# Kernel tuning notes

Hardware: AMD Instinct MI355X
Metric: run time of the kernel (lower is better)

The kernel has to match this reference:

```python
import jax, jax.numpy as jnp
import numpy as np

# Static tree-slice layout from TeaBlock.call:
# 15 windows of width 256 with stride 128 starting at 0, plus one window [1820:2176] (width 356).
_STARTS = np.arange(15) * 128  # starts for cores 1..15
_WIN_IDX = _STARTS[:, None] + np.arange(256)[None, :]  # (15, 256)
NUM_CLS = 10
NUM_OUT = round(256 / NUM_CLS) * NUM_CLS  # 260


def setup_inputs() -> dict:
    key = jax.random.key(0)
    ks = jax.random.split(key, 9)
    B = 16384
    s = 0.05
    return {
        "x":   jax.random.normal(ks[0], (B, 2176), dtype=jnp.float32),
        "W1":  jax.random.normal(ks[1], (15, 256, 64), dtype=jnp.float32) * s,
        "b1":  jnp.zeros((15, 64), dtype=jnp.float32),
        "W16": jax.random.normal(ks[2], (356, 64), dtype=jnp.float32) * s,
        "b16": jnp.zeros((64,), dtype=jnp.float32),
        "W2":  jax.random.normal(ks[3], (4, 256, 64), dtype=jnp.float32) * s,
        "b2":  jnp.zeros((4, 64), dtype=jnp.float32),
        "W3":  jax.random.normal(ks[4], (256, NUM_OUT), dtype=jnp.float32) * s,
        "b3":  jnp.zeros((NUM_OUT,), dtype=jnp.float32),
    }


def _tea(x, W, b):
    # Tea layer = constrained dense + ReLU (SNN-style accumulate-and-fire unit)
    return jax.nn.relu(x @ W + b)


def reference(x, W1, b1, W16, b16, W2, b2, W3, b3):
    B = x.shape[0]
    xf = x.reshape(B, -1)[:, :2176]
    # --- level 1: 15 regular strided windows, batched as one einsum ---
    xwin = xf[:, _WIN_IDX]                                   # (B, 15, 256)
    y15 = jax.nn.relu(jnp.einsum("bks,kso->bko", xwin, W1) + b1)  # (B, 15, 64)
    # core_1_16 on the irregular window [1820:2176]
    y16 = _tea(xf[:, 1820:2176], W16, b16)                   # (B, 64)
    # concat in original order x1..x16 -> (B, 1024), grouped 4-at-a-time into 256
    y = jnp.concatenate([y15.reshape(B, 15 * 64), y16], axis=1)  # (B, 1024)
    g = y.reshape(B, 4, 256)
    # --- level 2: 4 Tea(64), batched ---
    z = jax.nn.relu(jnp.einsum("bks,kso->bko", g, W2) + b2)  # (B, 4, 64)
    z = z.reshape(B, 256)
    # --- level 3: Tea(260) ---
    h = _tea(z, W3, b3)                                      # (B, 260)
    # AdditivePooling: sum NUM_OUT//NUM_CLS units per class
    pooled = h.reshape(B, NUM_CLS, NUM_OUT // NUM_CLS).sum(axis=2)  # (B, 10)
    return jax.nn.softmax(pooled, axis=-1)
```

## Files before the change

kernel.cpp:

```cpp
#include <hip/hip_runtime.h>
#include <cstdint>
#include <cstddef>

typedef _Float16 f16x8 __attribute__((ext_vector_type(8)));
typedef _Float16 f16x4 __attribute__((ext_vector_type(4)));
typedef float    f32x4 __attribute__((ext_vector_type(4)));

#define MFMA16(a,b,c) __builtin_amdgcn_mfma_f32_16x16x32_f16((a),(b),(c),0,0,0)

__global__ void tea_prep(const float* __restrict__ W1, const float* __restrict__ W16,
                         const float* __restrict__ W2, const float* __restrict__ W3,
                         _Float16* __restrict__ ws)
{
    int i = blockIdx.x * blockDim.x + threadIdx.x;
    if (i < 245760) {
        int win = i >> 14, t = i & 16383;
        int ot = t >> 12, kk = (t >> 9) & 7, l = (t >> 3) & 63, j = t & 7;
        int o = 16 * ot + (l & 15);
        int s = 32 * kk + 8 * (l >> 4) + j;
        ws[i] = (_Float16)W1[(win * 256 + s) * 64 + o];
    } else if (i < 270336) {
        int t = i - 245760;
        int ot = t / 6144, t2 = t % 6144;
        int kk = t2 >> 9, l = (t2 >> 3) & 63, j = t2 & 7;
        int o = 16 * ot + (l & 15);
        int sp = 32 * kk + 8 * (l >> 4) + j;
        ws[i] = (_Float16)((sp >= 12 && sp < 368) ? W16[(sp - 12) * 64 + o] : 0.f);
    } else if (i < 335872) {
        int t = i - 270336;
        int q2 = t >> 12, kk = (t >> 9) & 7, l = (t >> 3) & 63, j = t & 7;
        int og = 16 * q2 + (l & 15);
        int g = q2 >> 2, o2 = og - 64 * g;
        int s = 32 * kk + 8 * (l >> 4) + j;
        ws[i] = (_Float16)W2[(g * 256 + s) * 64 + o2];
    } else if (i < 405504) {
        int t = i - 335872;
        int tt = t >> 12, kk = (t >> 9) & 7, l = (t >> 3) & 63, j = t & 7;
        int o = 16 * tt + (l & 15);
        int s = 32 * kk + 8 * (l >> 4) + j;
        ws[i] = (_Float16)((o < 260) ? W3[s * 260 + o] : 0.f);
    }
}

__global__ __launch_bounds__(1024, 4)
void tea_dma(const float* __restrict__ x,
             const float* __restrict__ b1,  const float* __restrict__ b16,
             const float* __restrict__ b2,  const float* __restrict__ b3,
             const _Float16* __restrict__ ws, float* __restrict__ out)
{
    __shared__ _Float16 sh[74240];
    char* shb = (char*)sh;

    const int tid = threadIdx.x;
    const int bid = blockIdx.x;
    const int wg  = (bid & 7) * 64 + (bid >> 3);
    const int q = tid >> 6, l = tid & 63, r = l & 15, kg = l >> 4;
    const bool prod = (q >= 8);
    const int  pw   = q - 8;

    const char* xb = (const char*)(x + (size_t)wg * 32 * 2176);

    auto issue = [&](int c) {
        #pragma unroll
        for (int i = 0; i < 2; ++i) {
            int row = 4 * pw + 2 * i + (l >> 5);
            int colphys = (l & 31) * 16;
            int collog = colphys ^ ((row & 7) << 4);
            const void* src = xb + (size_t)row * 8704 + (size_t)c * 512 + collog;
            void* dst = shb + (c % 7) * 16384 + (4 * pw + 2 * i) * 512;
            __builtin_amdgcn_global_load_lds(
                (const __attribute__((address_space(1))) void*)src,
                (__attribute__((address_space(3))) void*)dst, 16, 0, 0);
        }
    };

#define PASSTOP(N) do { \
    if (prod) asm volatile("s_waitcnt vmcnt(" #N ")" ::: "memory"); \
    asm volatile("s_waitcnt lgkmcnt(0)" ::: "memory"); \
    __builtin_amdgcn_s_barrier(); \
    __builtin_amdgcn_sched_barrier(0); } while (0)
#define BARL() do { \
    asm volatile("s_waitcnt lgkmcnt(0)" ::: "memory"); \
    __builtin_amdgcn_s_barrier(); \
    __builtin_amdgcn_sched_barrier(0); } while (0)

    auto bfrag = [&](int slotbyte, int rowloc, int colb) -> f16x8 {
        int swz = (rowloc & 7) << 4;
        f32x4 u = *(const f32x4*)(shb + slotbyte + rowloc * 512 + (colb ^ swz));
        f32x4 v = *(const f32x4*)(shb + slotbyte + rowloc * 512 + ((colb + 16) ^ swz));
        f16x8 B;
        B[0] = (_Float16)u[0]; B[1] = (_Float16)u[1]; B[2] = (_Float16)u[2]; B[3] = (_Float16)u[3];
        B[4] = (_Float16)v[0]; B[5] = (_Float16)v[1]; B[6] = (_Float16)v[2]; B[7] = (_Float16)v[3];
        return B;
    };

    f16x8 Afn[8];
    if (!prod) {
        const _Float16* A0 = ws + (q >> 2) * 16384 + (q & 3) * 4096;
        #pragma unroll
        for (int kk = 0; kk < 8; ++kk)
            Afn[kk] = *(const f16x8*)(A0 + kk * 512 + l * 8);
    }

    auto wincomp2 = [&](int win, const float* bp, int nextwin) {
        float4 bv = *(const float4*)(bp + 16 * (q & 3) + 4 * kg);
        f32x4 acc0 = {0.f, 0.f, 0.f, 0.f}, acc1 = {0.f, 0.f, 0.f, 0.f};
        __builtin_amdgcn_s_setprio(1);
        #pragma unroll
        for (int kk = 0; kk < 8; ++kk) {
            int slotb = ((win + (kk >> 2)) % 7) * 16384;
            int colb = 128 * (kk & 3) + 32 * kg;
            f16x8 B0 = bfrag(slotb, r, colb);
            f16x8 B1 = bfrag(slotb, 16 + r, colb);
            acc0 = MFMA16(Afn[kk], B0, acc0);
            acc1 = MFMA16(Afn[kk], B1, acc1);
        }
        __builtin_amdgcn_s_setprio(0);
        if (nextwin >= 0) {
            const _Float16* An = ws + nextwin * 16384 + (q & 3) * 4096;
            #pragma unroll
            for (int kk = 0; kk < 8; ++kk)
                Afn[kk] = *(const f16x8*)(An + kk * 512 + l * 8);
        }
        f16x4 pk0, pk1;
        pk0[0] = (_Float16)fmaxf(acc0[0] + bv.x, 0.f);
        pk0[1] = (_Float16)fmaxf(acc0[1] + bv.y, 0.f);
        pk0[2] = (_Float16)fmaxf(acc0[2] + bv.z, 0.f);
        pk0[3] = (_Float16)fmaxf(acc0[3] + bv.w, 0.f);
        pk1[0] = (_Float16)fmaxf(acc1[0] + bv.x, 0.f);
        pk1[1] = (_Float16)fmaxf(acc1[1] + bv.y, 0.f);
        pk1[2] = (_Float16)fmaxf(acc1[2] + bv.z, 0.f);
        pk1[3] = (_Float16)fmaxf(acc1[3] + bv.w, 0.f);
        *(f16x4*)&sh[57344 + r * 264 + 64 * (win & 3) + 16 * (q & 3) + 4 * kg] = pk0;
        *(f16x4*)&sh[57344 + (16 + r) * 264 + 64 * (win & 3) + 16 * (q & 3) + 4 * kg] = pk1;
    };

    auto y16comp = [&](int rh) {
        const _Float16* A = ws + 245760 + (q & 3) * 6144;
        const int rowloc = 16 * rh + r;
        f32x4 acc = {0.f, 0.f, 0.f, 0.f};
        #pragma unroll
        for (int kk = 0; kk < 12; ++kk) {
            int off32 = 16 + 32 * kk + 8 * kg;
            if (32 * kk + 8 * kg >= 368) off32 = 376;
            int cc = off32 >> 7;
            int slotb = cc * 16384;
            int colb = (off32 & 127) * 4;
            f16x8 B  = bfrag(slotb, rowloc, colb);
            f16x8 Af = *(const f16x8*)(A + kk * 512 + l * 8);
            acc = MFMA16(Af, B, acc);
        }
        float4 bv = *(const float4*)(b16 + 16 * (q & 3) + 4 * kg);
        f16x4 pk;
        pk[0] = (_Float16)fmaxf(acc[0] + bv.x, 0.f);
        pk[1] = (_Float16)fmaxf(acc[1] + bv.y, 0.f);
        pk[2] = (_Float16)fmaxf(acc[2] + bv.z, 0.f);
        pk[3] = (_Float16)fmaxf(acc[3] + bv.w, 0.f);
        *(f16x4*)&sh[57344 + rowloc * 264 + 192 + 16 * (q & 3) + 4 * kg] = pk;
    };

    auto l2group = [&](int g) {
        if (q < 8) {
            int rh = q >> 2, t = 4 * g + (q & 3);
            const _Float16* A = ws + 270336 + t * 4096;
            f32x4 acc = {0.f, 0.f, 0.f, 0.f};
            #pragma unroll
            for (int kk = 0; kk < 8; ++kk) {
                f16x8 B  = *(const f16x8*)&sh[57344 + (16 * rh + r) * 264 + 32 * kk + 8 * kg];
                f16x8 Af = *(const f16x8*)(A + kk * 512 + l * 8);
                acc = MFMA16(Af, B, acc);
            }
            float4 bv = *(const float4*)(b2 + 16 * t + 4 * kg);
            f16x4 pk;
            pk[0] = (_Float16)fmaxf(acc[0] + bv.x, 0.f);
            pk[1] = (_Float16)fmaxf(acc[1] + bv.y, 0.f);
            pk[2] = (_Float16)fmaxf(acc[2] + bv.z, 0.f);
            pk[3] = (_Float16)fmaxf(acc[3] + bv.w, 0.f);
            *(f16x4*)&sh[65792 + (16 * rh + r) * 264 + 16 * t + 4 * kg] = pk;
        }
    };

    if (prod) { issue(0); issue(1); issue(2); issue(3); issue(4); }

    {
        const int wq = q >> 2;
        PASSTOP(4);
        if (prod) { issue(5); issue(6); }
        else      wincomp2(0 + wq, b1 + (0 + wq) * 64, 2 + wq);
        PASSTOP(4);
        if (prod) { issue(7); issue(8); }
        else      wincomp2(2 + wq, b1 + (2 + wq) * 64, 4 + wq);
        BARL(); l2group(0);
        PASSTOP(4);
        if (prod) { issue(9); issue(10); }
        else      wincomp2(4 + wq, b1 + (4 + wq) * 64, 6 + wq);
        PASSTOP(4);
        if (prod) { issue(11); issue(12); }
        else      wincomp2(6 + wq, b1 + (6 + wq) * 64, 8 + wq);
        BARL(); l2group(1);
        PASSTOP(4);
        if (prod) { issue(13); issue(14); }
        else      wincomp2(8 + wq, b1 + (8 + wq) * 64, 10 + wq);
        PASSTOP(4);
        if (prod) { issue(15); issue(16); }
        else      wincomp2(10 + wq, b1 + (10 + wq) * 64, 12 + wq);
        BARL(); l2group(2);
        PASSTOP(4);
        if (!prod) wincomp2(12 + wq, b1 + (12 + wq) * 64, -1);
        PASSTOP(0);
        if (!prod) {
            {
                const _Float16* A = ws + 14 * 16384 + (q & 3) * 4096;
                const int rh = q >> 2, rowloc = 16 * rh + r;
                f32x4 acc = {0.f, 0.f, 0.f, 0.f};
                #pragma unroll
                for (int kk = 0; kk < 8; ++kk) {
                    int slotb = ((14 + (kk >> 2)) % 7) * 16384;
                    int colb = 128 * (kk & 3) + 32 * kg;
                    f16x8 Af = *(const f16x8*)(A + kk * 512 + l * 8);
                    acc = MFMA16(Af, bfrag(slotb, rowloc, colb), acc);
                }
                float4 bv = *(const float4*)(b1 + 14 * 64 + 16 * (q & 3) + 4 * kg);
                f16x4 pk;
                pk[0] = (_Float16)fmaxf(acc[0] + bv.x, 0.f);
                pk[1] = (_Float16)fmaxf(acc[1] + bv.y, 0.f);
                pk[2] = (_Float16)fmaxf(acc[2] + bv.z, 0.f);
                pk[3] = (_Float16)fmaxf(acc[3] + bv.w, 0.f);
                *(f16x4*)&sh[57344 + rowloc * 264 + 64 * (14 & 3) + 16 * (q & 3) + 4 * kg] = pk;
            }
            y16comp(q >> 2);
        }
        BARL(); l2group(3);
    }
    BARL();

    {
        float* psp = (float*)sh;
        auto l3job = [&](int t, int rh2) {
            const _Float16* A = ws + 335872 + t * 4096;
            f32x4 acc = {0.f, 0.f, 0.f, 0.f};
            #pragma unroll
            for (int kk = 0; kk < 8; ++kk) {
                f16x8 B  = *(const f16x8*)&sh[65792 + (16 * rh2 + r) * 264 + 32 * kk + 8 * kg];
                f16x8 Af = *(const f16x8*)(A + kk * 512 + l * 8);
                acc = MFMA16(Af, B, acc);
            }
            float p[10];
            #pragma unroll
            for (int c = 0; c < 10; ++c) p[c] = 0.f;
            #pragma unroll
            for (int tt = 0; tt < 4; ++tt) {
                int o = 16 * t + 4 * kg + tt;
                if (o < 260) p[(unsigned)o / 26u] += fmaxf(acc[tt] + b3[o], 0.f);
            }
            #pragma unroll
            for (int c = 0; c < 10; ++c) {
                p[c] += __shfl_xor(p[c], 16);
                p[c] += __shfl_xor(p[c], 32);
            }
            if (kg == 0) {
                #pragma unroll
                for (int c = 0; c < 10; ++c)
                    psp[t * 320 + (16 * rh2 + r) * 10 + c] = p[c];
            }
        };
        l3job(q >> 1, q & 1);
        l3job((q + 16) >> 1, q & 1);
        if (q < 2) l3job(16, q);
    }
    BARL();

    if (tid < 32) {
        const float* psp = (const float*)sh;
        float v[10];
        #pragma unroll
        for (int c = 0; c < 10; ++c) {
            float s = 0.f;
            #pragma unroll
            for (int t = 0; t < 17; ++t) s += psp[t * 320 + tid * 10 + c];
            v[c] = s;
        }
        float mx = v[0];
        #pragma unroll
        for (int c = 1; c < 10; ++c) mx = fmaxf(mx, v[c]);
        float e[10], se = 0.f;
        #pragma unroll
        for (int c = 0; c < 10; ++c) { e[c] = expf(v[c] - mx); se += e[c]; }
        float inv = 1.f / se;
        float* orow = out + (size_t)(wg * 32 + tid) * 10;
        #pragma unroll
        for (int c = 0; c < 10; ++c) orow[c] = e[c] * inv;
    }
#undef PASSTOP
#undef BARL
}

extern "C" void kernel_launch(void* const* d_in, const int* in_sizes, int n_in,
                              void* d_out, int out_size, void* d_ws, size_t ws_size,
                              hipStream_t stream)
{
    const float* x   = (const float*)d_in[0];
    const float* W1  = (const float*)d_in[1];
    const float* b1  = (const float*)d_in[2];
    const float* W16 = (const float*)d_in[3];
    const float* b16 = (const float*)d_in[4];
    const float* W2  = (const float*)d_in[5];
    const float* b2  = (const float*)d_in[6];
    const float* W3  = (const float*)d_in[7];
    const float* b3  = (const float*)d_in[8];
    float*    out = (float*)d_out;
    _Float16* ws  = (_Float16*)d_ws;

    tea_prep<<<1584, 256, 0, stream>>>(W1, W16, W2, W3, ws);
    tea_dma <<<512, 1024, 0, stream>>>(x, b1, b16, b2, b3, ws, out);
}
```

Measured before the change: 62.35 us.

## Stage x through registers as fp16 and double rows per workgroup

Replaces the direct global-to-LDS async fp32 copies with register loads by producer waves that convert to fp16 before writing swizzled LDS slots. The fp16 staging halves LDS footprint per chunk, so each workgroup now processes 64 rows instead of 32 with a 5-slot ring, launching 256 blocks instead of 512. Intent is to cut LDS read and conversion work per MFMA and to reuse each weight fragment across four row tiles. The cost is an extra barrier-synchronised register stage, fewer blocks, and loss of the async DMA overlap.

Measured after the change: 51.18 us. 1.22x faster.

```diff
diff --git a/kernel.cpp b/kernel.cpp
--- a/kernel.cpp
+++ b/kernel.cpp
@@ -48,72 +48,82 @@
              const float* __restrict__ b2,  const float* __restrict__ b3,
              const _Float16* __restrict__ ws, float* __restrict__ out)
 {
-    __shared__ _Float16 sh[74240];
+    __shared__ _Float16 sh[74752];
     char* shb = (char*)sh;
 
     const int tid = threadIdx.x;
     const int bid = blockIdx.x;
-    const int wg  = (bid & 7) * 64 + (bid >> 3);
+    const int wg  = (bid & 7) * 32 + (bid >> 3);
     const int q = tid >> 6, l = tid & 63, r = l & 15, kg = l >> 4;
     const bool prod = (q >= 8);
     const int  pw   = q - 8;
 
-    const char* xb = (const char*)(x + (size_t)wg * 32 * 2176);
-
-    auto issue = [&](int c) {
-        #pragma unroll
-        for (int i = 0; i < 2; ++i) {
-            int row = 4 * pw + 2 * i + (l >> 5);
-            int colphys = (l & 31) * 16;
-            int collog = colphys ^ ((row & 7) << 4);
-            const void* src = xb + (size_t)row * 8704 + (size_t)c * 512 + collog;
-            void* dst = shb + (c % 7) * 16384 + (4 * pw + 2 * i) * 512;
-            __builtin_amdgcn_global_load_lds(
-                (const __attribute__((address_space(1))) void*)src,
-                (__attribute__((address_space(3))) void*)dst, 16, 0, 0);
-        }
-    };
-
-#define PASSTOP(N) do { \
-    if (prod) asm volatile("s_waitcnt vmcnt(" #N ")" ::: "memory"); \
-    asm volatile("s_waitcnt lgkmcnt(0)" ::: "memory"); \
-    __builtin_amdgcn_s_barrier(); \
-    __builtin_amdgcn_sched_barrier(0); } while (0)
+    const float* xf = x + (size_t)wg * 64 * 2176;
+
+    float4 SE[4], SO[4];
+    const int prow = 8 * pw + (l >> 3);
+    const int pcol = (l & 7) * 16;
+
+    auto pload = [&](int c, float4* S) {
+        const float* p = xf + (size_t)prow * 2176 + c * 128 + pcol;
+        S[0] = *(const float4*)(p);
+        S[1] = *(const float4*)(p + 4);
+        S[2] = *(const float4*)(p + 8);
+        S[3] = *(const float4*)(p + 12);
+    };
+    auto pwrite = [&](int c, float4* S) {
+        const int swz  = (prow & 15) << 4;
+        const int colb = pcol * 2;
+        char* base = shb + (c % 5) * 16384 + prow * 256;
+        f16x8 h0, h1;
+        h0[0]=(_Float16)S[0].x; h0[1]=(_Float16)S[0].y; h0[2]=(_Float16)S[0].z; h0[3]=(_Float16)S[0].w;
+        h0[4]=(_Float16)S[1].x; h0[5]=(_Float16)S[1].y; h0[6]=(_Float16)S[1].z; h0[7]=(_Float16)S[1].w;
+        h1[0]=(_Float16)S[2].x; h1[1]=(_Float16)S[2].y; h1[2]=(_Float16)S[2].z; h1[3]=(_Float16)S[2].w;
+        h1[4]=(_Float16)S[3].x; h1[5]=(_Float16)S[3].y; h1[6]=(_Float16)S[3].z; h1[7]=(_Float16)S[3].w;
+        *(f16x8*)(base + (colb ^ swz))        = h0;
+        *(f16x8*)(base + ((colb + 16) ^ swz)) = h1;
+    };
+
 #define BARL() do { \
     asm volatile("s_waitcnt lgkmcnt(0)" ::: "memory"); \
     __builtin_amdgcn_s_barrier(); \
     __builtin_amdgcn_sched_barrier(0); } while (0)
 
-    auto bfrag = [&](int slotbyte, int rowloc, int colb) -> f16x8 {
-        int swz = (rowloc & 7) << 4;
-        f32x4 u = *(const f32x4*)(shb + slotbyte + rowloc * 512 + (colb ^ swz));
-        f32x4 v = *(const f32x4*)(shb + slotbyte + rowloc * 512 + ((colb + 16) ^ swz));
-        f16x8 B;
-        B[0] = (_Float16)u[0]; B[1] = (_Float16)u[1]; B[2] = (_Float16)u[2]; B[3] = (_Float16)u[3];
-        B[4] = (_Float16)v[0]; B[5] = (_Float16)v[1]; B[6] = (_Float16)v[2]; B[7] = (_Float16)v[3];
-        return B;
+    auto bfrag = [&](int slotb, int rowloc, int colb) -> f16x8 {
+        int swz = (rowloc & 15) << 4;
+        return *(const f16x8*)(shb + slotb + rowloc * 256 + (colb ^ swz));
     };
 
     f16x8 Afn[8];
+    const int wq = q >> 2;
     if (!prod) {
-        const _Float16* A0 = ws + (q >> 2) * 16384 + (q & 3) * 4096;
+        const _Float16* A0 = ws + wq * 16384 + (q & 3) * 4096;
         #pragma unroll
         for (int kk = 0; kk < 8; ++kk)
             Afn[kk] = *(const f16x8*)(A0 + kk * 512 + l * 8);
     }
 
-    auto wincomp2 = [&](int win, const float* bp, int nextwin) {
+    auto ystore = [&](int rh, int winp, f32x4 a, float4 bv) {
+        f16x4 pk;
+        pk[0] = (_Float16)fmaxf(a[0] + bv.x, 0.f);
+        pk[1] = (_Float16)fmaxf(a[1] + bv.y, 0.f);
+        pk[2] = (_Float16)fmaxf(a[2] + bv.z, 0.f);
+        pk[3] = (_Float16)fmaxf(a[3] + bv.w, 0.f);
+        *(f16x4*)&sh[40960 + (16 * rh + r) * 264 + 64 * winp + 16 * (q & 3) + 4 * kg] = pk;
+    };
+
+    auto wincomp = [&](int win, const float* bp, int nextwin) {
         float4 bv = *(const float4*)(bp + 16 * (q & 3) + 4 * kg);
-        f32x4 acc0 = {0.f, 0.f, 0.f, 0.f}, acc1 = {0.f, 0.f, 0.f, 0.f};
+        f32x4 a0 = {0.f,0.f,0.f,0.f}, a1 = a0, a2 = a0, a3 = a0;
         __builtin_amdgcn_s_setprio(1);
         #pragma unroll
         for (int kk = 0; kk < 8; ++kk) {
-            int slotb = ((win + (kk >> 2)) % 7) * 16384;
-            int colb = 128 * (kk & 3) + 32 * kg;
-            f16x8 B0 = bfrag(slotb, r, colb);
-            f16x8 B1 = bfrag(slotb, 16 + r, colb);
-            acc0 = MFMA16(Afn[kk], B0, acc0);
-            acc1 = MFMA16(Afn[kk], B1, acc1);
+            int slotb = ((win + (kk >> 2)) % 5) * 16384;
+            int colb  = 64 * (kk & 3) + 16 * kg;
+            a0 = MFMA16(Afn[kk], bfrag(slotb,      r, colb), a0);
+            a1 = MFMA16(Afn[kk], bfrag(slotb, 16 + r, colb), a1);
+            a2 = MFMA16(Afn[kk], bfrag(slotb, 32 + r, colb), a2);
+            a3 = MFMA16(Afn[kk], bfrag(slotb, 48 + r, colb), a3);
         }
         __builtin_amdgcn_s_setprio(0);
         if (nextwin >= 0) {
@@ -122,126 +132,114 @@
             for (int kk = 0; kk < 8; ++kk)
                 Afn[kk] = *(const f16x8*)(An + kk * 512 + l * 8);
         }
-        f16x4 pk0, pk1;
-        pk0[0] = (_Float16)fmaxf(acc0[0] + bv.x, 0.f);
-        pk0[1] = (_Float16)fmaxf(acc0[1] + bv.y, 0.f);
-        pk0[2] = (_Float16)fmaxf(acc0[2] + bv.z, 0.f);
-        pk0[3] = (_Float16)fmaxf(acc0[3] + bv.w, 0.f);
-        pk1[0] = (_Float16)fmaxf(acc1[0] + bv.x, 0.f);
-        pk1[1] = (_Float16)fmaxf(acc1[1] + bv.y, 0.f);
-        pk1[2] = (_Float16)fmaxf(acc1[2] + bv.z, 0.f);
-        pk1[3] = (_Float16)fmaxf(acc1[3] + bv.w, 0.f);
-        *(f16x4*)&sh[57344 + r * 264 + 64 * (win & 3) + 16 * (q & 3) + 4 * kg] = pk0;
-        *(f16x4*)&sh[57344 + (16 + r) * 264 + 64 * (win & 3) + 16 * (q & 3) + 4 * kg] = pk1;
-    };
-
-    auto y16comp = [&](int rh) {
+        ystore(0, win & 3, a0, bv);
+        ystore(1, win & 3, a1, bv);
+        ystore(2, win & 3, a2, bv);
+        ystore(3, win & 3, a3, bv);
+    };
+
+    auto win14c = [&](int rh) {
+        float4 bv = *(const float4*)(b1 + 14 * 64 + 16 * (q & 3) + 4 * kg);
+        f32x4 acc = {0.f,0.f,0.f,0.f};
+        #pragma unroll
+        for (int kk = 0; kk < 8; ++kk) {
+            int slotb = ((14 + (kk >> 2)) % 5) * 16384;
+            int colb  = 64 * (kk & 3) + 16 * kg;
+            acc = MFMA16(Afn[kk], bfrag(slotb, 16 * rh + r, colb), acc);
+        }
+        ystore(rh, 2, acc, bv);
+    };
+
+    auto y16c = [&](int rh) {
         const _Float16* A = ws + 245760 + (q & 3) * 6144;
-        const int rowloc = 16 * rh + r;
-        f32x4 acc = {0.f, 0.f, 0.f, 0.f};
+        f32x4 acc = {0.f,0.f,0.f,0.f};
         #pragma unroll
         for (int kk = 0; kk < 12; ++kk) {
-            int off32 = 16 + 32 * kk + 8 * kg;
-            if (32 * kk + 8 * kg >= 368) off32 = 376;
-            int cc = off32 >> 7;
-            int slotb = cc * 16384;
-            int colb = (off32 & 127) * 4;
-            f16x8 B  = bfrag(slotb, rowloc, colb);
+            int offh = 16 + 32 * kk + 8 * kg;
+            if (32 * kk + 8 * kg >= 368) offh = 376;
+            int cc = offh >> 7;
+            int slotb = ((14 + cc) % 5) * 16384;
+            int colb  = (offh & 127) * 2;
             f16x8 Af = *(const f16x8*)(A + kk * 512 + l * 8);
-            acc = MFMA16(Af, B, acc);
+            acc = MFMA16(Af, bfrag(slotb, 16 * rh + r, colb), acc);
         }
         float4 bv = *(const float4*)(b16 + 16 * (q & 3) + 4 * kg);
-        f16x4 pk;
-        pk[0] = (_Float16)fmaxf(acc[0] + bv.x, 0.f);
-        pk[1] = (_Float16)fmaxf(acc[1] + bv.y, 0.f);
-        pk[2] = (_Float16)fmaxf(acc[2] + bv.z, 0.f);
-        pk[3] = (_Float16)fmaxf(acc[3] + bv.w, 0.f);
-        *(f16x4*)&sh[57344 + rowloc * 264 + 192 + 16 * (q & 3) + 4 * kg] = pk;
+        ystore(rh, 3, acc, bv);
     };
 
     auto l2group = [&](int g) {
         if (q < 8) {
-            int rh = q >> 2, t = 4 * g + (q & 3);
+            int t = 4 * g + (q & 3);
             const _Float16* A = ws + 270336 + t * 4096;
-            f32x4 acc = {0.f, 0.f, 0.f, 0.f};
-            #pragma unroll
-            for (int kk = 0; kk < 8; ++kk) {
-                f16x8 B  = *(const f16x8*)&sh[57344 + (16 * rh + r) * 264 + 32 * kk + 8 * kg];
-                f16x8 Af = *(const f16x8*)(A + kk * 512 + l * 8);
-                acc = MFMA16(Af, B, acc);
-            }
             float4 bv = *(const float4*)(b2 + 16 * t + 4 * kg);
-            f16x4 pk;
-            pk[0] = (_Float16)fmaxf(acc[0] + bv.x, 0.f);
-            pk[1] = (_Float16)fmaxf(acc[1] + bv.y, 0.f);
-            pk[2] = (_Float16)fmaxf(acc[2] + bv.z, 0.f);
-            pk[3] = (_Float16)fmaxf(acc[3] + bv.w, 0.f);
-            *(f16x4*)&sh[65792 + (16 * rh + r) * 264 + 16 * t + 4 * kg] = pk;
-        }
-    };
-
-    if (prod) { issue(0); issue(1); issue(2); issue(3); issue(4); }
-
-    {
-        const int wq = q >> 2;
-        PASSTOP(4);
-        if (prod) { issue(5); issue(6); }
-        else      wincomp2(0 + wq, b1 + (0 + wq) * 64, 2 + wq);
-        PASSTOP(4);
-        if (prod) { issue(7); issue(8); }
-        else      wincomp2(2 + wq, b1 + (2 + wq) * 64, 4 + wq);
-        BARL(); l2group(0);
-        PASSTOP(4);
-        if (prod) { issue(9); issue(10); }
-        else      wincomp2(4 + wq, b1 + (4 + wq) * 64, 6 + wq);
-        PASSTOP(4);
-        if (prod) { issue(11); issue(12); }
-        else      wincomp2(6 + wq, b1 + (6 + wq) * 64, 8 + wq);
-        BARL(); l2group(1);
-        PASSTOP(4);
-        if (prod) { issue(13); issue(14); }
-        else      wincomp2(8 + wq, b1 + (8 + wq) * 64, 10 + wq);
-        PASSTOP(4);
-        if (prod) { issue(15); issue(16); }
-        else      wincomp2(10 + wq, b1 + (10 + wq) * 64, 12 + wq);
-        BARL(); l2group(2);
-        PASSTOP(4);
-        if (!prod) wincomp2(12 + wq, b1 + (12 + wq) * 64, -1);
-        PASSTOP(0);
-        if (!prod) {
-            {
-                const _Float16* A = ws + 14 * 16384 + (q & 3) * 4096;
-                const int rh = q >> 2, rowloc = 16 * rh + r;
-                f32x4 acc = {0.f, 0.f, 0.f, 0.f};
+            #pragma unroll
+            for (int rr = 0; rr < 2; ++rr) {
+                int rh2 = (q >> 2) + 2 * rr;
+                f32x4 acc = {0.f,0.f,0.f,0.f};
                 #pragma unroll
                 for (int kk = 0; kk < 8; ++kk) {
-                    int slotb = ((14 + (kk >> 2)) % 7) * 16384;
-                    int colb = 128 * (kk & 3) + 32 * kg;
+                    f16x8 B  = *(const f16x8*)&sh[40960 + (16 * rh2 + r) * 264 + 32 * kk + 8 * kg];
                     f16x8 Af = *(const f16x8*)(A + kk * 512 + l * 8);
-                    acc = MFMA16(Af, bfrag(slotb, rowloc, colb), acc);
+                    acc = MFMA16(Af, B, acc);
                 }
-                float4 bv = *(const float4*)(b1 + 14 * 64 + 16 * (q & 3) + 4 * kg);
                 f16x4 pk;
                 pk[0] = (_Float16)fmaxf(acc[0] + bv.x, 0.f);
                 pk[1] = (_Float16)fmaxf(acc[1] + bv.y, 0.f);
                 pk[2] = (_Float16)fmaxf(acc[2] + bv.z, 0.f);
                 pk[3] = (_Float16)fmaxf(acc[3] + bv.w, 0.f);
-                *(f16x4*)&sh[57344 + rowloc * 264 + 64 * (14 & 3) + 16 * (q & 3) + 4 * kg] = pk;
-            }
-            y16comp(q >> 2);
-        }
-        BARL(); l2group(3);
-    }
+                *(f16x4*)&sh[57856 + (16 * rh2 + r) * 264 + 16 * t + 4 * kg] = pk;
+            }
+        }
+    };
+
+    if (prod) {
+        pload(0, SE); pload(1, SO);
+        pwrite(0, SE); pwrite(1, SO);
+        pload(2, SE); pload(3, SO);
+        pwrite(2, SE);
+        pload(4, SE);
+    }
+
+    BARL();
+    if (prod) { pwrite(3, SO); pwrite(4, SE); pload(5, SO); pload(6, SE); }
+    else      wincomp(wq, b1 + wq * 64, 2 + wq);
+    BARL();
+    if (prod) { pwrite(5, SO); pwrite(6, SE); pload(7, SO); pload(8, SE); }
+    else      wincomp(2 + wq, b1 + (2 + wq) * 64, 4 + wq);
+    BARL(); l2group(0);
+    BARL();
+    if (prod) { pwrite(7, SO); pwrite(8, SE); pload(9, SO); pload(10, SE); }
+    else      wincomp(4 + wq, b1 + (4 + wq) * 64, 6 + wq);
+    BARL();
+    if (prod) { pwrite(9, SO); pwrite(10, SE); pload(11, SO); pload(12, SE); }
+    else      wincomp(6 + wq, b1 + (6 + wq) * 64, 8 + wq);
+    BARL(); l2group(1);
+    BARL();
+    if (prod) { pwrite(11, SO); pwrite(12, SE); pload(13, SO); pload(14, SE); }
+    else      wincomp(8 + wq, b1 + (8 + wq) * 64, 10 + wq);
+    BARL();
+    if (prod) { pwrite(13, SO); pwrite(14, SE); pload(15, SO); pload(16, SE); }
+    else      wincomp(10 + wq, b1 + (10 + wq) * 64, 12 + wq);
+    BARL(); l2group(2);
+    BARL();
+    if (prod) { pwrite(15, SO); pwrite(16, SE); }
+    else      wincomp(12 + wq, b1 + (12 + wq) * 64, 14);
+    BARL();
+    if (!prod) {
+        win14c(q >> 2); win14c(2 + (q >> 2));
+        y16c(q >> 2);   y16c(2 + (q >> 2));
+    }
+    BARL(); l2group(3);
     BARL();
 
     {
         float* psp = (float*)sh;
         auto l3job = [&](int t, int rh2) {
             const _Float16* A = ws + 335872 + t * 4096;
-            f32x4 acc = {0.f, 0.f, 0.f, 0.f};
+            f32x4 acc = {0.f,0.f,0.f,0.f};
             #pragma unroll
             for (int kk = 0; kk < 8; ++kk) {
-                f16x8 B  = *(const f16x8*)&sh[65792 + (16 * rh2 + r) * 264 + 32 * kk + 8 * kg];
+                f16x8 B  = *(const f16x8*)&sh[57856 + (16 * rh2 + r) * 264 + 32 * kk + 8 * kg];
                 f16x8 Af = *(const f16x8*)(A + kk * 512 + l * 8);
                 acc = MFMA16(Af, B, acc);
             }
@@ -261,23 +259,25 @@
             if (kg == 0) {
                 #pragma unroll
                 for (int c = 0; c < 10; ++c)
-                    psp[t * 320 + (16 * rh2 + r) * 10 + c] = p[c];
+                    psp[t * 640 + (16 * rh2 + r) * 10 + c] = p[c];
             }
         };
-        l3job(q >> 1, q & 1);
-        l3job((q + 16) >> 1, q & 1);
-        if (q < 2) l3job(16, q);
-    }
-    BARL();
-
-    if (tid < 32) {
+        l3job((q >> 2),      q & 3);
+        l3job(4 + (q >> 2),  q & 3);
+        l3job(8 + (q >> 2),  q & 3);
+        l3job(12 + (q >> 2), q & 3);
+        if (q < 4) l3job(16, q);
+    }
+    BARL();
+
+    if (tid < 64) {
         const float* psp = (const float*)sh;
         float v[10];
         #pragma unroll
         for (int c = 0; c < 10; ++c) {
             float s = 0.f;
             #pragma unroll
-            for (int t = 0; t < 17; ++t) s += psp[t * 320 + tid * 10 + c];
+            for (int t = 0; t < 17; ++t) s += psp[t * 640 + tid * 10 + c];
             v[c] = s;
         }
         float mx = v[0];
@@ -287,11 +287,10 @@
         #pragma unroll
         for (int c = 0; c < 10; ++c) { e[c] = expf(v[c] - mx); se += e[c]; }
         float inv = 1.f / se;
-        float* orow = out + (size_t)(wg * 32 + tid) * 10;
+        float* orow = out + (size_t)(wg * 64 + tid) * 10;
         #pragma unroll
         for (int c = 0; c < 10; ++c) orow[c] = e[c] * inv;
     }
-#undef PASSTOP
 #undef BARL
 }
 
@@ -312,5 +311,5 @@
     _Float16* ws  = (_Float16*)d_ws;
 
     tea_prep<<<1584, 256, 0, stream>>>(W1, W16, W2, W3, ws);
-    tea_dma <<<512, 1024, 0, stream>>>(x, b1, b16, b2, b3, ws, out);
+    tea_dma <<<256, 1024, 0, stream>>>(x, b1, b16, b2, b3, ws, out);
 }
```
